# Performance work log

Hardware: AMD Instinct MI355X
Metric: run time of the kernel (lower is better)

Reference implementation:

```python
import jax, jax.numpy as jnp
import numpy as np


def _conv(x, w, b=None, pad=0):
    # x: [B,C,H,W], w: [O,I,kh,kw]
    y = jax.lax.conv_general_dilated(
        x, w, window_strides=(1, 1), padding=[(pad, pad), (pad, pad)],
        dimension_numbers=('NCHW', 'OIHW', 'NCHW'))
    if b is not None:
        y = y + b[None, :, None, None]
    return y


def _resb(x, w1, w2):
    h = _conv(x, w1, pad=1)
    h = jax.nn.leaky_relu(h, 0.1)
    h = _conv(h, w2, pad=1)
    return h + x


def setup_inputs() -> dict:
    key = jax.random.key(0)
    ks = jax.random.split(key, 16)
    B, C, H, W, K = 2, 64, 128, 256, 16
    s = 0.05
    return {
        'x_left': jax.random.normal(ks[0], (B, C, H, W), jnp.float32),
        'x_right': jax.random.normal(ks[1], (B, C, H, W), jnp.float32),
        'xxs': jax.random.randint(ks[2], (B, H * W, K), 0, H, jnp.int32),
        'yys': jax.random.randint(ks[3], (B, H * W, K), 0, W, jnp.int32),
        'is_training': 0,
        'rb_w1': jax.random.normal(ks[4], (C, C, 3, 3), jnp.float32) * s,
        'rb_w2': jax.random.normal(ks[5], (C, C, 3, 3), jnp.float32) * s,
        'b1_w': jax.random.normal(ks[6], (C, C, 1, 1), jnp.float32) * s,
        'b1_b': jax.random.normal(ks[7], (C,), jnp.float32) * s,
        'b2_w': jax.random.normal(ks[8], (C, C, 1, 1), jnp.float32) * s,
        'b2_b': jax.random.normal(ks[9], (C,), jnp.float32) * s,
        'b3_w': jax.random.normal(ks[10], (C, C, 1, 1), jnp.float32) * s,
        'b3_b': jax.random.normal(ks[11], (C,), jnp.float32) * s,
        'fus_w': jax.random.normal(ks[12], (C, 2 * C, 1, 1), jnp.float32) * s,
        'fus_b': jax.random.normal(ks[13], (C,), jnp.float32) * s,
    }


def reference(x_left, x_right, xxs, yys, is_training,
              rb_w1, rb_w2, b1_w, b1_b, b2_w, b2_b, b3_w, b3_b, fus_w, fus_b):
    B, C, H, W = x_left.shape
    HW = H * W
    K = xxs.shape[-1]

    buf_l = _resb(x_left, rb_w1, rb_w2)
    buf_r = _resb(x_right, rb_w1, rb_w2)

    Q = _conv(buf_l, b1_w, b1_b)   # [B,C,H,W]
    S = _conv(buf_r, b2_w, b2_b)
    R = _conv(buf_r, b3_w, b3_b)

    # per-pixel gather: S[b,:,Pos_x,Pos_y] -> flat index into H*W
    flat = (xxs.astype(jnp.int32) * W + yys.astype(jnp.int32)).reshape(B, HW * K)  # [B,HW*K]
    Sf = S.reshape(B, C, HW)
    Rf = R.reshape(B, C, HW)
    Key = jnp.take_along_axis(Sf, flat[:, None, :], axis=2).reshape(B, C, HW, K)
    Val = jnp.take_along_axis(Rf, flat[:, None, :], axis=2).reshape(B, C, HW, K)

    Qv = Q.transpose(0, 2, 3, 1).reshape(B, HW, C)           # [B,HW,C]
    score = jnp.einsum('bpc,bcpk->bpk', Qv, Key)             # [B,HW,K]
    M = jax.nn.softmax(score, axis=-1)                       # [B,HW,K]
    buf = jnp.einsum('bpk,bckp->bpc', M, Val.transpose(0, 1, 3, 2))  # [B,HW,C]
    buf = buf.reshape(B, H, W, C).transpose(0, 3, 1, 2)      # [B,C,H,W]

    out = _conv(jnp.concatenate([buf, x_left], axis=1), fus_w, fus_b)
    M_right_to_left = M[:, :, None, :]                       # [B,HW,1,K] as in torch
    if is_training == 1:
        return out
    return (out, M_right_to_left)
```

## Files before the change

kernel.cpp:

```cpp
#include <hip/hip_runtime.h>

#define HH 128
#define WW 256
#define CH 64
#define HWP (HH * WW)

typedef __attribute__((ext_vector_type(8))) __bf16 bf16x8;
typedef __attribute__((ext_vector_type(16))) float float16;

__device__ __forceinline__ unsigned short f2bf(float f) {
    unsigned u = __float_as_uint(f);
    u += 0x7fffu + ((u >> 16) & 1u);
    return (unsigned short)(u >> 16);
}
__device__ __forceinline__ float bf2f(unsigned short u) {
    return __uint_as_float((unsigned)u << 16);
}
template <int CTRL>
__device__ __forceinline__ float dpp_add(float x) {
    int t = __builtin_amdgcn_update_dpp(0, __float_as_int(x), CTRL, 0xF, 0xF, true);
    return x + __int_as_float(t);
}

__global__ __launch_bounds__(256) void prep_toT_k(
    const float* __restrict__ xl, const float* __restrict__ xr,
    const float* __restrict__ w1, const float* __restrict__ w2,
    const float* __restrict__ b1w, const float* __restrict__ b2w,
    const float* __restrict__ b3w, const float* __restrict__ fusw,
    unsigned short* __restrict__ XT, unsigned short* __restrict__ wB)
{
    const int tid = threadIdx.x;
    if (blockIdx.x < 2048) {
        __shared__ __align__(16) unsigned short sT[64 * 68];
        const int side = blockIdx.x >> 10;
        const int i0   = blockIdx.x & 1023;
        const int gp0  = i0 * 64;
        const int b    = gp0 >> 15;
        const int pofs = gp0 & (HWP - 1);
        const float* in = (side ? xr : xl) + (size_t)b * CH * HWP + pofs;

        for (int i = tid; i < 4096; i += 256) {
            int ci = i >> 6, px = i & 63;
            sT[px * 68 + ci] = f2bf(in[(size_t)ci * HWP + px]);
        }
        __syncthreads();
        const int px = tid >> 2, q = tid & 3;
        unsigned short* op = XT + ((size_t)(side * 2 + b) * HWP + pofs + px) * 64;
#pragma unroll
        for (int r = 0; r < 2; ++r)
            *(uint4*)&op[(q * 2 + r) * 8] = *(uint4*)&sT[px * 68 + (q * 2 + r) * 8];
        return;
    }

    int e = (blockIdx.x - 2048) * 256 + tid;
    float val;
    if (e < 73728) {
        const float* w = (e < 36864) ? w1 : w2;
        int t = (e < 36864) ? e : e - 36864;
        int j = t & 7, L = (t >> 3) & 63, nb = (t >> 9) & 1, kc = t >> 10;
        int k  = kc * 16 + (L >> 5) * 8 + j;
        int n  = nb * 32 + (L & 31);
        int kd = k >> 6, ci = k & 63;
        val = w[(n * 64 + ci) * 9 + kd];
    } else {
        int t = e - 73728;
        if (t < 4096) {
            int j = t & 7, L = (t >> 3) & 63, i3 = t >> 9;
            int nt = i3 & 1, kc = i3 >> 1;
            int n = nt * 32 + (L & 31), k = kc * 16 + (L >> 5) * 8 + j;
            val = b1w[n * 64 + k];
        } else if (t < 12288) {
            t -= 4096;
            int j = t & 7, L = (t >> 3) & 63, i3 = t >> 9;
            int nt = i3 & 3, kc = i3 >> 2;
            int n = nt * 32 + (L & 31), k = kc * 16 + (L >> 5) * 8 + j;
            val = (n < 64) ? b2w[n * 64 + k] : b3w[(n - 64) * 64 + k];
        } else {
            t -= 12288;
            int j = t & 7, L = (t >> 3) & 63, i3 = t >> 9;
            int nt = i3 & 1, kc = i3 >> 1;
            int n = nt * 32 + (L & 31), k = kc * 16 + (L >> 5) * 8 + j;
            val = fusw[n * 128 + k];
        }
    }
    wB[e] = f2bf(val);
}

__device__ __forceinline__ void stage_halo4(
    unsigned short* sA, const unsigned short* inT, int x0, int y0, int tid)
{
    for (int i = tid; i < 2112; i += 512) {
        int cell = i >> 3, j = i & 7;
        int row = cell / 66, col = cell - row * 66;
        int gy = y0 + row - 1, gx = x0 + col - 1;
        uint4 v = make_uint4(0, 0, 0, 0);
        if ((unsigned)gy < HH && (unsigned)gx < WW)
            v = *(const uint4*)&inT[(size_t)(gy * WW + gx) * 64 + j * 8];
        *(uint4*)&sA[(row * 66 + col) * 68 + j * 8] = v;
    }
}

__global__ __launch_bounds__(512) void conv1_k(
    const unsigned short* __restrict__ XT, const unsigned short* __restrict__ wB,
    unsigned short* __restrict__ H1T)
{
    __shared__ __align__(16) unsigned short sA[4 * 66 * 68];

    const int tid = threadIdx.x;
    const int x0  = blockIdx.x * 64;
    const int y0  = blockIdx.y * 2;
    const int sb  = blockIdx.z;
    const unsigned short* inT = XT + (size_t)sb * HWP * 64;

    stage_halo4(sA, inT, x0, y0, tid);
    __syncthreads();

    const int lane = tid & 63, wv = tid >> 6;
    const int rr = wv & 1, mw = (wv >> 1) & 1, nw = wv >> 2;
    const int m = lane & 31, kg = lane >> 5;
    const int pxl = mw * 32 + m;

    float16 acc;
#pragma unroll
    for (int i = 0; i < 16; ++i) acc[i] = 0.f;

#pragma unroll
    for (int kc = 0; kc < 36; ++kc) {
        const int kd = kc >> 2, hh = kc & 3;
        const int dy = kd / 3, dx = kd - dy * 3;
        bf16x8 af = *(const bf16x8*)&sA[((rr + dy) * 66 + pxl + dx) * 68 + hh * 16 + kg * 8];
        bf16x8 bf = *(const bf16x8*)&wB[((kc * 2 + nw) * 64 + lane) * 8];
        acc = __builtin_amdgcn_mfma_f32_32x32x16_bf16(af, bf, acc, 0, 0, 0);
    }

    __syncthreads();
    unsigned short* sCb = sA;
    const int n = nw * 32 + (lane & 31);
#pragma unroll
    for (int r = 0; r < 16; ++r) {
        int pr = rr * 64 + mw * 32 + (r & 3) + 8 * (r >> 2) + 4 * kg;
        float v = acc[r];
        v = v > 0.f ? v : 0.1f * v;
        sCb[pr * 68 + n] = f2bf(v);
    }
    __syncthreads();

    const int px2 = tid >> 2, q = tid & 3;
    const int orow = px2 >> 6, px = px2 & 63;
    unsigned short* op = H1T + ((size_t)sb * HWP + (y0 + orow) * WW + x0 + px) * 64 + q * 16;
    *(uint4*)&op[0] = *(uint4*)&sCb[px2 * 68 + q * 16];
    *(uint4*)&op[8] = *(uint4*)&sCb[px2 * 68 + q * 16 + 8];
}

__global__ __launch_bounds__(512) void conv2_k(
    const unsigned short* __restrict__ H1T, const unsigned short* __restrict__ XT,
    const unsigned short* __restrict__ wB2, const unsigned short* __restrict__ wQ,
    const unsigned short* __restrict__ wSR, const float* __restrict__ b1b,
    const float* __restrict__ b2b, const float* __restrict__ b3b,
    unsigned short* __restrict__ QT, unsigned short* __restrict__ ST,
    unsigned short* __restrict__ RT)
{
    __shared__ __align__(16) unsigned short sA[4 * 66 * 68];

    const int tid = threadIdx.x;
    const int x0  = blockIdx.x * 64;
    const int y0  = blockIdx.y * 2;
    const int sb  = blockIdx.z;
    const int side = sb >> 1, b = sb & 1;
    const unsigned short* inT = H1T + (size_t)sb * HWP * 64;

    stage_halo4(sA, inT, x0, y0, tid);
    __syncthreads();

    const int lane = tid & 63, wv = tid >> 6;
    const int rr = wv & 1, mw = (wv >> 1) & 1, nw = wv >> 2;
    const int m = lane & 31, kg = lane >> 5;
    const int pxl = mw * 32 + m;

    float16 acc;
#pragma unroll
    for (int i = 0; i < 16; ++i) acc[i] = 0.f;

#pragma unroll
    for (int kc = 0; kc < 36; ++kc) {
        const int kd = kc >> 2, hh = kc & 3;
        const int dy = kd / 3, dx = kd - dy * 3;
        bf16x8 af = *(const bf16x8*)&sA[((rr + dy) * 66 + pxl + dx) * 68 + hh * 16 + kg * 8];
        bf16x8 bf = *(const bf16x8*)&wB2[((kc * 2 + nw) * 64 + lane) * 8];
        acc = __builtin_amdgcn_mfma_f32_32x32x16_bf16(af, bf, acc, 0, 0, 0);
    }

    __syncthreads();
    unsigned short* sCb = sA;
    unsigned short* sC2 = sA + 8704;
    const int n = nw * 32 + (lane & 31);
    const unsigned short* xres = XT + (size_t)sb * HWP * 64;
#pragma unroll
    for (int r = 0; r < 16; ++r) {
        int pr = rr * 64 + mw * 32 + (r & 3) + 8 * (r >> 2) + 4 * kg;
        float xv = bf2f(xres[(size_t)((y0 + (pr >> 6)) * WW + x0 + (pr & 63)) * 64 + n]);
        sCb[pr * 68 + n] = f2bf(acc[r] + xv);
    }
    __syncthreads();

    const int px2 = tid >> 2, q = tid & 3;
    const int orow = px2 >> 6, px = px2 & 63;
    const size_t prow = (size_t)b * HWP + (y0 + orow) * WW + x0 + px;

    if (side == 0) {
        float16 a2;
#pragma unroll
        for (int i = 0; i < 16; ++i) a2[i] = 0.f;
#pragma unroll
        for (int kc = 0; kc < 4; ++kc) {
            bf16x8 af = *(const bf16x8*)&sCb[(rr * 64 + pxl) * 68 + kc * 16 + kg * 8];
            bf16x8 bf = *(const bf16x8*)&wQ[((kc * 2 + nw) * 64 + lane) * 8];
            a2 = __builtin_amdgcn_mfma_f32_32x32x16_bf16(af, bf, a2, 0, 0, 0);
        }
        float bv = b1b[n];
#pragma unroll
        for (int r = 0; r < 16; ++r) {
            int pr = rr * 64 + mw * 32 + (r & 3) + 8 * (r >> 2) + 4 * kg;
            sC2[pr * 68 + n] = f2bf(a2[r] + bv);
        }
        __syncthreads();
        unsigned short* op = QT + prow * 64 + q * 16;
        *(uint4*)&op[0] = *(uint4*)&sC2[px2 * 68 + q * 16];
        *(uint4*)&op[8] = *(uint4*)&sC2[px2 * 68 + q * 16 + 8];
    } else {
        float16 a2;
#pragma unroll
        for (int i = 0; i < 16; ++i) a2[i] = 0.f;
#pragma unroll
        for (int kc = 0; kc < 4; ++kc) {
            bf16x8 af = *(const bf16x8*)&sCb[(rr * 64 + pxl) * 68 + kc * 16 + kg * 8];
            bf16x8 bf = *(const bf16x8*)&wSR[((kc * 4 + nw) * 64 + lane) * 8];
            a2 = __builtin_amdgcn_mfma_f32_32x32x16_bf16(af, bf, a2, 0, 0, 0);
        }
        {
            float bv = b2b[n];
#pragma unroll
            for (int r = 0; r < 16; ++r) {
                int pr = rr * 64 + mw * 32 + (r & 3) + 8 * (r >> 2) + 4 * kg;
                sC2[pr * 68 + n] = f2bf(a2[r] + bv);
            }
        }
        __syncthreads();
        {
            unsigned short* op = ST + prow * 64 + q * 16;
            *(uint4*)&op[0] = *(uint4*)&sC2[px2 * 68 + q * 16];
            *(uint4*)&op[8] = *(uint4*)&sC2[px2 * 68 + q * 16 + 8];
        }
        __syncthreads();

#pragma unroll
        for (int i = 0; i < 16; ++i) a2[i] = 0.f;
#pragma unroll
        for (int kc = 0; kc < 4; ++kc) {
            bf16x8 af = *(const bf16x8*)&sCb[(rr * 64 + pxl) * 68 + kc * 16 + kg * 8];
            bf16x8 bf = *(const bf16x8*)&wSR[((kc * 4 + 2 + nw) * 64 + lane) * 8];
            a2 = __builtin_amdgcn_mfma_f32_32x32x16_bf16(af, bf, a2, 0, 0, 0);
        }
        {
            float bv = b3b[n];
#pragma unroll
            for (int r = 0; r < 16; ++r) {
                int pr = rr * 64 + mw * 32 + (r & 3) + 8 * (r >> 2) + 4 * kg;
                sC2[pr * 68 + n] = f2bf(a2[r] + bv);
            }
        }
        __syncthreads();
        {
            unsigned short* op = RT + prow * 64 + q * 16;
            *(uint4*)&op[0] = *(uint4*)&sC2[px2 * 68 + q * 16];
            *(uint4*)&op[8] = *(uint4*)&sC2[px2 * 68 + q * 16 + 8];
        }
    }
}

__global__ __launch_bounds__(256) void attn_fuse_k(
    const unsigned short* __restrict__ QT, const unsigned short* __restrict__ ST,
    const unsigned short* __restrict__ RT, const int* __restrict__ xxs,
    const int* __restrict__ yys, const unsigned short* __restrict__ XT,
    const unsigned short* __restrict__ wfrag, const float* __restrict__ bias,
    float* __restrict__ out, float* __restrict__ Mout)
{
    __shared__ __align__(16) unsigned char smem[9216];
    unsigned short* sBuf = (unsigned short*)smem;
    unsigned short* sXT  = (unsigned short*)smem + 32 * 68;
    float*          sC   = (float*)smem;

    const int tid  = threadIdx.x;
    const int lane = tid & 63;
    const int wv   = tid >> 6;

    const int blk = blockIdx.x;
    const int b   = (blk & 4) ? 1 : 0;
    const int sub = (blk >> 3) * 4 + (blk & 3);
    const int pofs = sub * 32;
    const size_t gp0   = (size_t)b * HWP + pofs;
    const size_t bbase = (size_t)b * HWP;

    {
        const unsigned short* xlT = XT + gp0 * 64;
        int px = tid >> 3, j = tid & 7;
        *(uint4*)&sXT[px * 68 + j * 8] = *(const uint4*)&xlT[(size_t)px * 64 + j * 8];
    }

    const int k  = lane & 15, cq = lane >> 4;
    const unsigned short* rbase = RT + bbase * 64;
    const unsigned short* sbase = ST + bbase * 64;

    size_t gp = gp0 + wv * 8;
    int flat = xxs[gp * 16 + k] * WW + yys[gp * 16 + k];

    for (int it = 0; it < 8; ++it) {
        int nflat = 0;
        if (it < 7)
            nflat = xxs[(gp + 1) * 16 + k] * WW + yys[(gp + 1) * 16 + k];

        uint4 sv0 = *(const uint4*)(sbase + (size_t)flat * 64 + cq * 16);
        uint4 sv1 = *(const uint4*)(sbase + (size_t)flat * 64 + cq * 16 + 8);
        uint4 qv0 = *(const uint4*)(QT + gp * 64 + cq * 16);
        uint4 qv1 = *(const uint4*)(QT + gp * 64 + cq * 16 + 8);

        unsigned short rv[16];
#pragma unroll
        for (int kk = 0; kk < 16; ++kk) {
            int fi = __builtin_amdgcn_readlane(flat, kk);
            rv[kk] = rbase[((unsigned)fi << 6) + lane];
        }

        float s0 = 0.f, s1 = 0.f;
        {
            const unsigned* sa  = (const unsigned*)&sv0;
            const unsigned* qa  = (const unsigned*)&qv0;
            const unsigned* sb2 = (const unsigned*)&sv1;
            const unsigned* qb2 = (const unsigned*)&qv1;
#pragma unroll
            for (int d = 0; d < 4; ++d) {
                s0 = fmaf(__uint_as_float(sa[d] << 16),
                          __uint_as_float(qa[d] << 16), s0);
                s0 = fmaf(__uint_as_float(sa[d] & 0xffff0000u),
                          __uint_as_float(qa[d] & 0xffff0000u), s0);
                s1 = fmaf(__uint_as_float(sb2[d] << 16),
                          __uint_as_float(qb2[d] << 16), s1);
                s1 = fmaf(__uint_as_float(sb2[d] & 0xffff0000u),
                          __uint_as_float(qb2[d] & 0xffff0000u), s1);
            }
        }
        float s = s0 + s1;
        s += __shfl_xor(s, 16, 64);
        s += __shfl_xor(s, 32, 64);

        const float e = __expf(s);

        float acc0 = 0.f, acc1 = 0.f;
#pragma unroll
        for (int kk = 0; kk < 8; ++kk) {
            float ea = __uint_as_float(
                __builtin_amdgcn_readlane(__float_as_uint(e), kk));
            float eb = __uint_as_float(
                __builtin_amdgcn_readlane(__float_as_uint(e), kk + 8));
            acc0 = fmaf(ea, bf2f(rv[kk]), acc0);
            acc1 = fmaf(eb, bf2f(rv[kk + 8]), acc1);
        }

        float sum = e;
        sum = dpp_add<0xB1>(sum);
        sum = dpp_add<0x4E>(sum);
        sum = dpp_add<0x141>(sum);
        sum = dpp_add<0x140>(sum);
        const float rinv = 1.f / sum;

        if (lane < 16) Mout[gp * 16 + lane] = e * rinv;
        sBuf[(wv * 8 + it) * 68 + lane] = f2bf((acc0 + acc1) * rinv);

        flat = nflat;
        ++gp;
    }
    __syncthreads();

    float16 facc;
#pragma unroll
    for (int i = 0; i < 16; ++i) facc[i] = 0.f;
    const int nw = wv;
    const int kg = lane >> 5;
    const int px_l = lane & 31;

    if (tid < 128) {
#pragma unroll
        for (int kc = 0; kc < 8; ++kc) {
            const unsigned short* asrc = (kc < 4)
                ? &sBuf[px_l * 68 + kc * 16 + kg * 8]
                : &sXT[px_l * 68 + (kc - 4) * 16 + kg * 8];
            bf16x8 af = *(const bf16x8*)asrc;
            bf16x8 bf = *(const bf16x8*)&wfrag[((kc * 2 + nw) * 64 + lane) * 8];
            facc = __builtin_amdgcn_mfma_f32_32x32x16_bf16(af, bf, facc, 0, 0, 0);
        }
    }
    __syncthreads();

    if (tid < 128) {
        const int co_l = nw * 32 + (lane & 31);
#pragma unroll
        for (int r = 0; r < 16; ++r) {
            int pr = (r & 3) + 8 * (r >> 2) + 4 * kg;
            sC[co_l * 36 + pr] = facc[r];
        }
    }
    __syncthreads();

    {
        const int co = tid >> 2, p0 = (tid & 3) * 8;
        const float bv = bias[co];
        float* op = out + ((size_t)b * CH + co) * HWP + pofs + p0;
#pragma unroll
        for (int q = 0; q < 2; ++q) {
            float4 v = *(float4*)&sC[co * 36 + p0 + q * 4];
            v.x += bv; v.y += bv; v.z += bv; v.w += bv;
            *(float4*)&op[q * 4] = v;
        }
    }
}

extern "C" void kernel_launch(void* const* d_in, const int* in_sizes, int n_in,
                              void* d_out, int out_size, void* d_ws, size_t ws_size,
                              hipStream_t stream)
{
    const float* x_left  = (const float*)d_in[0];
    const float* x_right = (const float*)d_in[1];
    const int*   xxs     = (const int*)d_in[2];
    const int*   yys     = (const int*)d_in[3];
    const float* rb_w1   = (const float*)d_in[5];
    const float* rb_w2   = (const float*)d_in[6];
    const float* b1_w    = (const float*)d_in[7];
    const float* b1_b    = (const float*)d_in[8];
    const float* b2_w    = (const float*)d_in[9];
    const float* b2_b    = (const float*)d_in[10];
    const float* b3_w    = (const float*)d_in[11];
    const float* b3_b    = (const float*)d_in[12];
    const float* fus_w   = (const float*)d_in[13];
    const float* fus_b   = (const float*)d_in[14];

    float* out  = (float*)d_out;
    float* Mout = out + (size_t)2 * CH * HWP;

    unsigned short* ws2 = (unsigned short*)d_ws;
    unsigned short* XT   = ws2;
    unsigned short* H1T  = ws2 + 8388608;
    unsigned short* QT   = ws2 + 16777216;
    unsigned short* ST   = ws2 + 20971520;
    unsigned short* RT   = ws2 + 25165824;
    unsigned short* wB   = ws2 + 29360128;

    prep_toT_k<<<2416, 256, 0, stream>>>(x_left, x_right, rb_w1, rb_w2,
                                         b1_w, b2_w, b3_w, fus_w, XT, wB);

    conv1_k<<<dim3(4, 64, 4), 512, 0, stream>>>(XT, wB, H1T);
    conv2_k<<<dim3(4, 64, 4), 512, 0, stream>>>(H1T, XT, wB + 36864, wB + 73728,
                                                wB + 77824, b1_b, b2_b, b3_b,
                                                QT, ST, RT);

    attn_fuse_k<<<2048, 256, 0, stream>>>(QT, ST, RT, xxs, yys, XT,
                                          wB + 86016, fus_b, out, Mout);
}
```

Measured before the change: 189.9 us.

## Vectorize prep loads, remap conv blocks per XCD, interleave S/R MFMA chains

The prep transpose now reads inputs as float4 and scatters four bf16 values into shared memory, where before it did scalar loads. The conv kernels switch to a 1D grid whose decode sends contiguous row bands of the image to the same XCD, so halo rows are more likely to be reused in that XCD's L2. In conv2, the S and R 1x1 projections share their A-fragment loads and run as two interleaved MFMA accumulator chains, hiding dependency latency. The cost is more register pressure from the second accumulator and extra shared-memory bank conflicts from the scattered transpose writes.

```diff
diff --git a/kernel.cpp b/kernel.cpp
--- a/kernel.cpp
+++ b/kernel.cpp
@@ -39,9 +39,13 @@
         const int pofs = gp0 & (HWP - 1);
         const float* in = (side ? xr : xl) + (size_t)b * CH * HWP + pofs;
 
-        for (int i = tid; i < 4096; i += 256) {
-            int ci = i >> 6, px = i & 63;
-            sT[px * 68 + ci] = f2bf(in[(size_t)ci * HWP + px]);
+        for (int i = tid; i < 1024; i += 256) {
+            int ci = i >> 4, p4 = (i & 15) * 4;
+            float4 v = *(const float4*)&in[(size_t)ci * HWP + p4];
+            sT[(p4 + 0) * 68 + ci] = f2bf(v.x);
+            sT[(p4 + 1) * 68 + ci] = f2bf(v.y);
+            sT[(p4 + 2) * 68 + ci] = f2bf(v.z);
+            sT[(p4 + 3) * 68 + ci] = f2bf(v.w);
         }
         __syncthreads();
         const int px = tid >> 2, q = tid & 3;
@@ -100,6 +104,16 @@
     }
 }
 
+__device__ __forceinline__ void conv_decode(int wg, int& sb, int& x0, int& y0)
+{
+    const int xcd = wg & 7, r = wg >> 3;
+    sb = r >> 5;
+    const int u = r & 31;
+    const int by = xcd * 8 + (u >> 2), bx = u & 3;
+    x0 = bx * 64;
+    y0 = by * 2;
+}
+
 __global__ __launch_bounds__(512) void conv1_k(
     const unsigned short* __restrict__ XT, const unsigned short* __restrict__ wB,
     unsigned short* __restrict__ H1T)
@@ -107,9 +121,8 @@
     __shared__ __align__(16) unsigned short sA[4 * 66 * 68];
 
     const int tid = threadIdx.x;
-    const int x0  = blockIdx.x * 64;
-    const int y0  = blockIdx.y * 2;
-    const int sb  = blockIdx.z;
+    int sb, x0, y0;
+    conv_decode(blockIdx.x, sb, x0, y0);
     const unsigned short* inT = XT + (size_t)sb * HWP * 64;
 
     stage_halo4(sA, inT, x0, y0, tid);
@@ -163,9 +176,8 @@
     __shared__ __align__(16) unsigned short sA[4 * 66 * 68];
 
     const int tid = threadIdx.x;
-    const int x0  = blockIdx.x * 64;
-    const int y0  = blockIdx.y * 2;
-    const int sb  = blockIdx.z;
+    int sb, x0, y0;
+    conv_decode(blockIdx.x, sb, x0, y0);
     const int side = sb >> 1, b = sb & 1;
     const unsigned short* inT = H1T + (size_t)sb * HWP * 64;
 
@@ -228,22 +240,22 @@
         *(uint4*)&op[0] = *(uint4*)&sC2[px2 * 68 + q * 16];
         *(uint4*)&op[8] = *(uint4*)&sC2[px2 * 68 + q * 16 + 8];
     } else {
-        float16 a2;
-#pragma unroll
-        for (int i = 0; i < 16; ++i) a2[i] = 0.f;
+        float16 aS, aR;
+#pragma unroll
+        for (int i = 0; i < 16; ++i) { aS[i] = 0.f; aR[i] = 0.f; }
 #pragma unroll
         for (int kc = 0; kc < 4; ++kc) {
             bf16x8 af = *(const bf16x8*)&sCb[(rr * 64 + pxl) * 68 + kc * 16 + kg * 8];
-            bf16x8 bf = *(const bf16x8*)&wSR[((kc * 4 + nw) * 64 + lane) * 8];
-            a2 = __builtin_amdgcn_mfma_f32_32x32x16_bf16(af, bf, a2, 0, 0, 0);
-        }
-        {
-            float bv = b2b[n];
-#pragma unroll
-            for (int r = 0; r < 16; ++r) {
-                int pr = rr * 64 + mw * 32 + (r & 3) + 8 * (r >> 2) + 4 * kg;
-                sC2[pr * 68 + n] = f2bf(a2[r] + bv);
-            }
+            bf16x8 bS = *(const bf16x8*)&wSR[((kc * 4 + nw) * 64 + lane) * 8];
+            bf16x8 bR = *(const bf16x8*)&wSR[((kc * 4 + 2 + nw) * 64 + lane) * 8];
+            aS = __builtin_amdgcn_mfma_f32_32x32x16_bf16(af, bS, aS, 0, 0, 0);
+            aR = __builtin_amdgcn_mfma_f32_32x32x16_bf16(af, bR, aR, 0, 0, 0);
+        }
+        const float bvS = b2b[n], bvR = b3b[n];
+#pragma unroll
+        for (int r = 0; r < 16; ++r) {
+            int pr = rr * 64 + mw * 32 + (r & 3) + 8 * (r >> 2) + 4 * kg;
+            sC2[pr * 68 + n] = f2bf(aS[r] + bvS);
         }
         __syncthreads();
         {
@@ -252,22 +264,10 @@
             *(uint4*)&op[8] = *(uint4*)&sC2[px2 * 68 + q * 16 + 8];
         }
         __syncthreads();
-
-#pragma unroll
-        for (int i = 0; i < 16; ++i) a2[i] = 0.f;
-#pragma unroll
-        for (int kc = 0; kc < 4; ++kc) {
-            bf16x8 af = *(const bf16x8*)&sCb[(rr * 64 + pxl) * 68 + kc * 16 + kg * 8];
-            bf16x8 bf = *(const bf16x8*)&wSR[((kc * 4 + 2 + nw) * 64 + lane) * 8];
-            a2 = __builtin_amdgcn_mfma_f32_32x32x16_bf16(af, bf, a2, 0, 0, 0);
-        }
-        {
-            float bv = b3b[n];
-#pragma unroll
-            for (int r = 0; r < 16; ++r) {
-                int pr = rr * 64 + mw * 32 + (r & 3) + 8 * (r >> 2) + 4 * kg;
-                sC2[pr * 68 + n] = f2bf(a2[r] + bv);
-            }
+#pragma unroll
+        for (int r = 0; r < 16; ++r) {
+            int pr = rr * 64 + mw * 32 + (r & 3) + 8 * (r >> 2) + 4 * kg;
+            sC2[pr * 68 + n] = f2bf(aR[r] + bvR);
         }
         __syncthreads();
         {
@@ -457,10 +457,10 @@
     prep_toT_k<<<2416, 256, 0, stream>>>(x_left, x_right, rb_w1, rb_w2,
                                          b1_w, b2_w, b3_w, fus_w, XT, wB);
 
-    conv1_k<<<dim3(4, 64, 4), 512, 0, stream>>>(XT, wB, H1T);
-    conv2_k<<<dim3(4, 64, 4), 512, 0, stream>>>(H1T, XT, wB + 36864, wB + 73728,
-                                                wB + 77824, b1_b, b2_b, b3_b,
-                                                QT, ST, RT);
+    conv1_k<<<1024, 512, 0, stream>>>(XT, wB, H1T);
+    conv2_k<<<1024, 512, 0, stream>>>(H1T, XT, wB + 36864, wB + 73728,
+                                      wB + 77824, b1_b, b2_b, b3_b,
+                                      QT, ST, RT);
 
     attn_fuse_k<<<2048, 256, 0, stream>>>(QT, ST, RT, xxs, yys, XT,
                                           wB + 86016, fus_b, out, Mout);
```

Measured after the change: 187.8 us (median of 2 runs). No clear change (-1.1%).
